# Optimization experiments

Hardware: AMD Instinct MI355X
Metric: run time of the kernel (lower is better)

## Reference

```python
import jax, jax.numpy as jnp
import numpy as np
from jax import lax

K = 5
SCALE = 100.0
IN_CHN = 128
OUT_CHN = 128
KS = 3
STRIDE = 1
PAD = 1
N_W = OUT_CHN * IN_CHN * KS * KS


def setup_inputs() -> dict:
    key = jax.random.key(0)
    k1, k2, k3, k4, k5 = jax.random.split(key, 5)
    x = jax.random.normal(k1, (32, IN_CHN, 56, 56), dtype=jnp.float32)
    Alpha = jax.random.uniform(k2, (OUT_CHN, 1, 1), dtype=jnp.float32)
    # xavier-normal-ish init for M, Z
    M = jax.random.normal(k3, (OUT_CHN, IN_CHN, KS, KS), dtype=jnp.float32) * 0.05
    Z = jax.random.normal(k4, (K, OUT_CHN, IN_CHN, KS, KS), dtype=jnp.float32) * 0.05
    # rv ~ N(0, 1/sqrt(scale)) of shape (1, K); sample is all-zeros so the random branch is taken
    rv = jax.random.normal(k5, (1, K), dtype=jnp.float32) / np.float32(np.sqrt(SCALE))
    return {"x": x, "Alpha": Alpha, "M": M, "Z": Z, "rv": rv}


def reference(x, Alpha, M, Z, rv):
    # --- SDP weight synthesis (normalization is done under no_grad in torch) ---
    m = M.reshape(N_W)                # (N,)
    z = Z.reshape(K, N_W)             # (K, N)
    A = m * m + jnp.sum(z * z, axis=0) / SCALE
    inv = lax.rsqrt(A)
    m_n = m * inv
    z_n = z * inv
    w = (rv @ z_n + m_n).reshape(OUT_CHN, IN_CHN, KS, KS)  # (O,I,k,k)
    # --- sign binarization of weights and activations (ReCU) ---
    bw = jnp.sign(w)
    ba = jnp.sign(x)
    # --- conv2d, NCHW/OIHW ---
    out = lax.conv_general_dilated(
        ba, bw,
        window_strides=(STRIDE, STRIDE),
        padding=[(PAD, PAD), (PAD, PAD)],
        dimension_numbers=("NCHW", "OIHW", "NCHW"),
    )
    out = out * Alpha  # Alpha (O,1,1) broadcasts over (B,O,H,W)
    return out
```

## Files before the change

### kernel.cpp

```cpp
#include <hip/hip_runtime.h>
#include <stdint.h>

typedef unsigned int u32;
typedef unsigned long long u64;

#define HW      3136
#define PADW    58
#define PADHW   3364

#define WB_OFF   0
#define BF_OFF   18432
#define N2A_OFF  23040
#define AB_OFF   23552

#define NB_W     128
#define NB_A     392
#define NB_R     29

__global__ __launch_bounds__(256) void k_prep(
    const float* __restrict__ x, const float* __restrict__ Alpha,
    const float* __restrict__ M, const float* __restrict__ Z,
    const float* __restrict__ rv, char* __restrict__ ws)
{
  int t = threadIdx.x;
  if (blockIdx.x < NB_W) {
    u32*   wb  = (u32*)(ws + WB_OFF);
    float* Bf  = (float*)(ws + BF_OFF);
    float* n2a = (float*)(ws + N2A_OFF);
    __shared__ float sw[1152];
    __shared__ u32 sbits[36];
    __shared__ int spc[9];
    int o = blockIdx.x;
    float r0 = rv[0], r1 = rv[1], r2 = rv[2], r3 = rv[3], r4 = rv[4];
    const float4* M4 = (const float4*)M;
    const float4* Z4 = (const float4*)Z;
    float4* sw4 = (float4*)sw;

    for (int j = t; j < 288; j += 256) {
      float4 a = M4[o * 288 + j];
      float4 z;
      z = Z4[0 * 36864 + o * 288 + j];
      a.x = fmaf(r0, z.x, a.x); a.y = fmaf(r0, z.y, a.y);
      a.z = fmaf(r0, z.z, a.z); a.w = fmaf(r0, z.w, a.w);
      z = Z4[1 * 36864 + o * 288 + j];
      a.x = fmaf(r1, z.x, a.x); a.y = fmaf(r1, z.y, a.y);
      a.z = fmaf(r1, z.z, a.z); a.w = fmaf(r1, z.w, a.w);
      z = Z4[2 * 36864 + o * 288 + j];
      a.x = fmaf(r2, z.x, a.x); a.y = fmaf(r2, z.y, a.y);
      a.z = fmaf(r2, z.z, a.z); a.w = fmaf(r2, z.w, a.w);
      z = Z4[3 * 36864 + o * 288 + j];
      a.x = fmaf(r3, z.x, a.x); a.y = fmaf(r3, z.y, a.y);
      a.z = fmaf(r3, z.z, a.z); a.w = fmaf(r3, z.w, a.w);
      z = Z4[4 * 36864 + o * 288 + j];
      a.x = fmaf(r4, z.x, a.x); a.y = fmaf(r4, z.y, a.y);
      a.z = fmaf(r4, z.z, a.z); a.w = fmaf(r4, z.w, a.w);
      sw4[j] = a;
    }
    __syncthreads();

    if (t < 36) {
      int tap = t >> 2;
      int wd  = t & 3;
      u32 bits = 0;
#pragma unroll
      for (int c = 0; c < 32; ++c) {
        float v = sw[(wd * 32 + c) * 9 + tap];
        bits |= (v > 0.0f ? 1u : 0u) << c;
      }
      wb[(o * 9 + tap) * 4 + wd] = bits;
      sbits[t] = bits;
    }
    __syncthreads();
    if (t < 9)
      spc[t] = __popc(sbits[4 * t]) + __popc(sbits[4 * t + 1])
             + __popc(sbits[4 * t + 2]) + __popc(sbits[4 * t + 3]);
    __syncthreads();
    if (t < 9) {
      int ht = t / 3, wt = t - ht * 3;
      int corr = 0;
#pragma unroll
      for (int tap = 0; tap < 9; ++tap) {
        int dh = tap / 3, dw = tap - dh * 3;
        int inv = ((ht == 0) & (dh == 0)) | ((ht == 2) & (dh == 2)) |
                  ((wt == 0) & (dw == 0)) | ((wt == 2) & (dw == 2));
        if (inv) corr += 128 - 2 * spc[tap];
      }
      Bf[t * 128 + o] = (float)(1152 - corr) * Alpha[o];
    }
    if (t == 0) n2a[o] = -2.0f * Alpha[o];
  } else if (blockIdx.x < NB_W + NB_A) {
    u32* abw = (u32*)(ws + AB_OFF);
    int idx = (blockIdx.x - NB_W) * 256 + t;
    int bg  = idx / 784;
    int q   = idx - bg * 784;
    int b   = bg >> 2;
    int g   = bg & 3;
    int h   = q / 14;
    int w0  = (q - h * 14) * 4;

    const float4* X4 = (const float4*)x
        + ((size_t)b * 128 + g * 32) * (HW / 4) + q;
    u32 m0 = 0, m1 = 0, m2 = 0, m3 = 0;
#pragma unroll
    for (int c = 0; c < 32; ++c) {
      float4 f = X4[(size_t)c * (HW / 4)];
      m0 |= (f.x > 0.0f ? 1u : 0u) << c;
      m1 |= (f.y > 0.0f ? 1u : 0u) << c;
      m2 |= (f.z > 0.0f ? 1u : 0u) << c;
      m3 |= (f.w > 0.0f ? 1u : 0u) << c;
    }
    size_t base = ((size_t)b * PADHW + (h + 1) * PADW + (w0 + 1)) * 4 + g;
    abw[base]      = m0;
    abw[base + 4]  = m1;
    abw[base + 8]  = m2;
    abw[base + 12] = m3;
  } else {
    uint4* ab4 = (uint4*)(ws + AB_OFF);
    int e = (blockIdx.x - NB_W - NB_A) * 256 + t;
    if (e >= 32 * 228) return;
    int b  = e / 228;
    int r  = e - b * 228;
    int pp;
    if      (r < 58)  pp = r;
    else if (r < 116) pp = 57 * PADW + (r - 58);
    else {
      int s = r - 116;
      pp = (1 + (s >> 1)) * PADW + ((s & 1) ? 57 : 0);
    }
    ab4[(size_t)b * PADHW + pp] = make_uint4(0, 0, 0, 0);
  }
}

__global__ __launch_bounds__(256) void k_conv(
    const char* __restrict__ ws, float* __restrict__ out)
{
  const uint4* ab   = (const uint4*)(ws + AB_OFF);
  const u32*   wbw  = (const u32*)(ws + WB_OFF);
  const float* BfG  = (const float*)(ws + BF_OFF);
  const float* n2aG = (const float*)(ws + N2A_OFF);

  __shared__ float sBf[9][16];
  int t  = threadIdx.x;
  int o0 = blockIdx.y * 16;
  if (t < 144)
    (&sBf[0][0])[t] = BfG[(t >> 4) * 128 + o0 + (t & 15)];
  __syncthreads();

  int gp = blockIdx.x * 256 + t;
  int b  = gp / HW;
  int p  = gp - b * HW;
  int h  = p / 56;
  int w  = p - h * 56;

  const uint4* ap = ab + (size_t)b * PADHW + (size_t)h * PADW + w;
  u32 A[9][4];
#pragma unroll
  for (int rr = 0; rr < 3; ++rr)
#pragma unroll
    for (int cc = 0; cc < 3; ++cc) {
      uint4 v = ap[(size_t)rr * PADW + cc];
      A[rr * 3 + cc][0] = v.x; A[rr * 3 + cc][1] = v.y;
      A[rr * 3 + cc][2] = v.z; A[rr * 3 + cc][3] = v.w;
    }

  int cl = ((h == 0) ? 0 : (h == 55 ? 6 : 3))
         + ((w == 0) ? 0 : (w == 55 ? 2 : 1));

  float* outp = out + ((size_t)b * 128 + o0) * HW + p;

#pragma unroll 2
  for (int oi = 0; oi < 16; ++oi) {
    const u32* wp = wbw + (size_t)(o0 + oi) * 36;
    int s = 0;
#pragma unroll
    for (int tap = 0; tap < 9; ++tap) {
      s += __popc(A[tap][0] ^ wp[tap * 4 + 0]);
      s += __popc(A[tap][1] ^ wp[tap * 4 + 1]);
      s += __popc(A[tap][2] ^ wp[tap * 4 + 2]);
      s += __popc(A[tap][3] ^ wp[tap * 4 + 3]);
    }
    float ov = fmaf((float)s, n2aG[o0 + oi], sBf[cl][oi]);
    __builtin_nontemporal_store(ov, outp + (size_t)oi * HW);
  }
}

extern "C" void kernel_launch(void* const* d_in, const int* in_sizes, int n_in,
                              void* d_out, int out_size, void* d_ws, size_t ws_size,
                              hipStream_t stream)
{
  const float* x     = (const float*)d_in[0];
  const float* Alpha = (const float*)d_in[1];
  const float* M     = (const float*)d_in[2];
  const float* Z     = (const float*)d_in[3];
  const float* rv    = (const float*)d_in[4];
  float* out         = (float*)d_out;
  char*  ws          = (char*)d_ws;

  k_prep<<<NB_W + NB_A + NB_R, 256, 0, stream>>>(x, Alpha, M, Z, rv, ws);
  k_conv<<<dim3(392, 8), 256, 0, stream>>>(ws, out);
}
```

Baseline: 138.4 us.

## Replace XNOR-popcount binary conv with int8 MFMA implicit GEMM

```diff
diff --git a/kernel.cpp b/kernel.cpp
--- a/kernel.cpp
+++ b/kernel.cpp
@@ -3,33 +3,28 @@
 
 typedef unsigned int u32;
 typedef unsigned long long u64;
+typedef int i32x4 __attribute__((ext_vector_type(4)));
 
 #define HW      3136
 #define PADW    58
 #define PADHW   3364
 
-#define WB_OFF   0
-#define BF_OFF   18432
-#define N2A_OFF  23040
-#define AB_OFF   23552
+#define WT_OFF   0
+#define AP_OFF   147456
+#define AP_IMG   (PADHW * 128)
 
 #define NB_W     128
 #define NB_A     392
 #define NB_R     29
 
 __global__ __launch_bounds__(256) void k_prep(
-    const float* __restrict__ x, const float* __restrict__ Alpha,
+    const float* __restrict__ x,
     const float* __restrict__ M, const float* __restrict__ Z,
     const float* __restrict__ rv, char* __restrict__ ws)
 {
   int t = threadIdx.x;
   if (blockIdx.x < NB_W) {
-    u32*   wb  = (u32*)(ws + WB_OFF);
-    float* Bf  = (float*)(ws + BF_OFF);
-    float* n2a = (float*)(ws + N2A_OFF);
     __shared__ float sw[1152];
-    __shared__ u32 sbits[36];
-    __shared__ int spc[9];
     int o = blockIdx.x;
     float r0 = rv[0], r1 = rv[1], r2 = rv[2], r3 = rv[3], r4 = rv[4];
     const float4* M4 = (const float4*)M;
@@ -58,38 +53,21 @@
     }
     __syncthreads();
 
-    if (t < 36) {
-      int tap = t >> 2;
-      int wd  = t & 3;
-      u32 bits = 0;
-#pragma unroll
-      for (int c = 0; c < 32; ++c) {
-        float v = sw[(wd * 32 + c) * 9 + tap];
-        bits |= (v > 0.0f ? 1u : 0u) << c;
+    u32* wt32 = (u32*)(ws + WT_OFF);
+    for (int j = t; j < 288; j += 256) {
+      u32 wword = 0;
+#pragma unroll
+      for (int k2 = 0; k2 < 4; ++k2) {
+        int i   = j * 4 + k2;
+        int tap = i >> 7;
+        int ch  = i & 127;
+        u32 bb = (sw[ch * 9 + tap] > 0.0f) ? 0x01u : 0xFFu;
+        wword |= bb << (k2 * 8);
       }
-      wb[(o * 9 + tap) * 4 + wd] = bits;
-      sbits[t] = bits;
-    }
-    __syncthreads();
-    if (t < 9)
-      spc[t] = __popc(sbits[4 * t]) + __popc(sbits[4 * t + 1])
-             + __popc(sbits[4 * t + 2]) + __popc(sbits[4 * t + 3]);
-    __syncthreads();
-    if (t < 9) {
-      int ht = t / 3, wt = t - ht * 3;
-      int corr = 0;
-#pragma unroll
-      for (int tap = 0; tap < 9; ++tap) {
-        int dh = tap / 3, dw = tap - dh * 3;
-        int inv = ((ht == 0) & (dh == 0)) | ((ht == 2) & (dh == 2)) |
-                  ((wt == 0) & (dw == 0)) | ((wt == 2) & (dw == 2));
-        if (inv) corr += 128 - 2 * spc[tap];
-      }
-      Bf[t * 128 + o] = (float)(1152 - corr) * Alpha[o];
-    }
-    if (t == 0) n2a[o] = -2.0f * Alpha[o];
+      wt32[o * 288 + j] = wword;
+    }
   } else if (blockIdx.x < NB_W + NB_A) {
-    u32* abw = (u32*)(ws + AB_OFF);
+    char* Ap = ws + AP_OFF;
     int idx = (blockIdx.x - NB_W) * 256 + t;
     int bg  = idx / 784;
     int q   = idx - bg * 784;
@@ -100,22 +78,34 @@
 
     const float4* X4 = (const float4*)x
         + ((size_t)b * 128 + g * 32) * (HW / 4) + q;
-    u32 m0 = 0, m1 = 0, m2 = 0, m3 = 0;
+    u32 pk[4][8];
+#pragma unroll
+    for (int px = 0; px < 4; ++px)
+#pragma unroll
+      for (int wi = 0; wi < 8; ++wi) pk[px][wi] = 0;
 #pragma unroll
     for (int c = 0; c < 32; ++c) {
       float4 f = X4[(size_t)c * (HW / 4)];
-      m0 |= (f.x > 0.0f ? 1u : 0u) << c;
-      m1 |= (f.y > 0.0f ? 1u : 0u) << c;
-      m2 |= (f.z > 0.0f ? 1u : 0u) << c;
-      m3 |= (f.w > 0.0f ? 1u : 0u) << c;
-    }
-    size_t base = ((size_t)b * PADHW + (h + 1) * PADW + (w0 + 1)) * 4 + g;
-    abw[base]      = m0;
-    abw[base + 4]  = m1;
-    abw[base + 8]  = m2;
-    abw[base + 12] = m3;
+      int wi = c >> 2, sh = (c & 3) * 8;
+      u32 b0 = f.x > 0.0f ? 0x01u : 0xFFu;
+      u32 b1 = f.y > 0.0f ? 0x01u : 0xFFu;
+      u32 b2 = f.z > 0.0f ? 0x01u : 0xFFu;
+      u32 b3 = f.w > 0.0f ? 0x01u : 0xFFu;
+      pk[0][wi] |= b0 << sh;
+      pk[1][wi] |= b1 << sh;
+      pk[2][wi] |= b2 << sh;
+      pk[3][wi] |= b3 << sh;
+    }
+    size_t pbase = ((size_t)b * PADHW + (h + 1) * PADW + (w0 + 1)) * 128 + g * 32;
+#pragma unroll
+    for (int px = 0; px < 4; ++px) {
+      uint4 v0 = make_uint4(pk[px][0], pk[px][1], pk[px][2], pk[px][3]);
+      uint4 v1 = make_uint4(pk[px][4], pk[px][5], pk[px][6], pk[px][7]);
+      *(uint4*)(Ap + pbase + (size_t)px * 128)      = v0;
+      *(uint4*)(Ap + pbase + (size_t)px * 128 + 16) = v1;
+    }
   } else {
-    uint4* ab4 = (uint4*)(ws + AB_OFF);
+    char* Ap = ws + AP_OFF;
     int e = (blockIdx.x - NB_W - NB_A) * 256 + t;
     if (e >= 32 * 228) return;
     int b  = e / 228;
@@ -127,60 +117,73 @@
       int s = r - 116;
       pp = (1 + (s >> 1)) * PADW + ((s & 1) ? 57 : 0);
     }
-    ab4[(size_t)b * PADHW + pp] = make_uint4(0, 0, 0, 0);
+    char* p = Ap + ((size_t)b * PADHW + pp) * 128;
+    uint4 z = make_uint4(0, 0, 0, 0);
+#pragma unroll
+    for (int k = 0; k < 8; ++k) *(uint4*)(p + k * 16) = z;
   }
 }
 
-__global__ __launch_bounds__(256) void k_conv(
-    const char* __restrict__ ws, float* __restrict__ out)
+__global__ __launch_bounds__(512) void k_mm(
+    const char* __restrict__ ws, const float* __restrict__ Alpha,
+    float* __restrict__ out)
 {
-  const uint4* ab   = (const uint4*)(ws + AB_OFF);
-  const u32*   wbw  = (const u32*)(ws + WB_OFF);
-  const float* BfG  = (const float*)(ws + BF_OFF);
-  const float* n2aG = (const float*)(ws + N2A_OFF);
-
-  __shared__ float sBf[9][16];
-  int t  = threadIdx.x;
-  int o0 = blockIdx.y * 16;
-  if (t < 144)
-    (&sBf[0][0])[t] = BfG[(t >> 4) * 128 + o0 + (t & 15)];
-  __syncthreads();
-
-  int gp = blockIdx.x * 256 + t;
-  int b  = gp / HW;
-  int p  = gp - b * HW;
-  int h  = p / 56;
-  int w  = p - h * 56;
-
-  const uint4* ap = ab + (size_t)b * PADHW + (size_t)h * PADW + w;
-  u32 A[9][4];
-#pragma unroll
-  for (int rr = 0; rr < 3; ++rr)
-#pragma unroll
-    for (int cc = 0; cc < 3; ++cc) {
-      uint4 v = ap[(size_t)rr * PADW + cc];
-      A[rr * 3 + cc][0] = v.x; A[rr * 3 + cc][1] = v.y;
-      A[rr * 3 + cc][2] = v.z; A[rr * 3 + cc][3] = v.w;
-    }
-
-  int cl = ((h == 0) ? 0 : (h == 55 ? 6 : 3))
-         + ((w == 0) ? 0 : (w == 55 ? 2 : 1));
-
-  float* outp = out + ((size_t)b * 128 + o0) * HW + p;
-
-#pragma unroll 2
-  for (int oi = 0; oi < 16; ++oi) {
-    const u32* wp = wbw + (size_t)(o0 + oi) * 36;
-    int s = 0;
-#pragma unroll
-    for (int tap = 0; tap < 9; ++tap) {
-      s += __popc(A[tap][0] ^ wp[tap * 4 + 0]);
-      s += __popc(A[tap][1] ^ wp[tap * 4 + 1]);
-      s += __popc(A[tap][2] ^ wp[tap * 4 + 2]);
-      s += __popc(A[tap][3] ^ wp[tap * 4 + 3]);
-    }
-    float ov = fmaf((float)s, n2aG[o0 + oi], sBf[cl][oi]);
-    __builtin_nontemporal_store(ov, outp + (size_t)oi * HW);
+  const char* Wt = ws + WT_OFF;
+  const char* Ap = ws + AP_OFF;
+
+  int t   = threadIdx.x;
+  int wv  = t >> 6;
+  int l   = t & 63;
+  int l15 = l & 15;
+  int lk  = (l >> 4) * 16;
+  int o0  = wv * 16;
+
+  int blk = blockIdx.x;
+  int b   = blk / 28;
+  int rb  = blk - b * 28;
+  int h0  = rb * 2;
+
+  const char* apb = Ap + (size_t)b * AP_IMG;
+
+  int pp0[7];
+#pragma unroll
+  for (int n = 0; n < 7; ++n) {
+    int px = n * 16 + l15;
+    int r  = (px >= 56) ? 1 : 0;
+    pp0[n] = (h0 + r) * PADW + (px - r * 56);
+  }
+
+  i32x4 acc[7];
+#pragma unroll
+  for (int n = 0; n < 7; ++n) acc[n] = (i32x4){0, 0, 0, 0};
+
+  const char* wr = Wt + (size_t)(o0 + l15) * 1152 + lk;
+
+#pragma unroll
+  for (int tap = 0; tap < 9; ++tap) {
+    const int dh = tap / 3, dw = tap - (tap / 3) * 3;
+    const int sh = dh * PADW + dw;
+#pragma unroll
+    for (int kk = 0; kk < 2; ++kk) {
+      i32x4 af = *(const i32x4*)(wr + tap * 128 + kk * 64);
+#pragma unroll
+      for (int n = 0; n < 7; ++n) {
+        i32x4 bf = *(const i32x4*)(apb + (size_t)(pp0[n] + sh) * 128 + kk * 64 + lk);
+        acc[n] = __builtin_amdgcn_mfma_i32_16x16x64_i8(af, bf, acc[n], 0, 0, 0);
+      }
+    }
+  }
+
+  float4 al = *(const float4*)(Alpha + o0 + (l >> 4) * 4);
+  float* ob = out + ((size_t)b * 128 + o0 + (l >> 4) * 4) * HW + h0 * 56;
+#pragma unroll
+  for (int n = 0; n < 7; ++n) {
+    int px = n * 16 + l15;
+    float* op = ob + px;
+    __builtin_nontemporal_store((float)acc[n].x * al.x, op);
+    __builtin_nontemporal_store((float)acc[n].y * al.y, op + HW);
+    __builtin_nontemporal_store((float)acc[n].z * al.z, op + 2 * HW);
+    __builtin_nontemporal_store((float)acc[n].w * al.w, op + 3 * HW);
   }
 }
 
@@ -196,6 +199,6 @@
   float* out         = (float*)d_out;
   char*  ws          = (char*)d_ws;
 
-  k_prep<<<NB_W + NB_A + NB_R, 256, 0, stream>>>(x, Alpha, M, Z, rv, ws);
-  k_conv<<<dim3(392, 8), 256, 0, stream>>>(ws, out);
+  k_prep<<<NB_W + NB_A + NB_R, 256, 0, stream>>>(x, M, Z, rv, ws);
+  k_mm<<<32 * 28, 512, 0, stream>>>(ws, Alpha, out);
 }
```

Measured after the change: 240.3 us. +73.7%, slower.
